# Kernel tuning notes

Measured on AMD Instinct MI355X. Metric: run time of the kernel, lower is better.

Reference implementation:

```python
import jax, jax.numpy as jnp
import numpy as np

N_HEADS = 16
HEAD_DIM = 64
N_EMBD = 1024
B, S = 2, 2048


def setup_inputs() -> dict:
    key = jax.random.key(0)
    k1, k2, k3 = jax.random.split(key, 3)
    x = jax.random.normal(k1, (B, S, N_EMBD), dtype=jnp.float32)
    W_attn = jax.random.normal(k2, (N_EMBD, 3 * N_EMBD), dtype=jnp.float32) * 0.02
    b_attn = jnp.zeros((3 * N_EMBD,), dtype=jnp.float32)
    W_proj = jax.random.normal(k3, (N_EMBD, N_EMBD), dtype=jnp.float32) * 0.02
    b_proj = jnp.zeros((N_EMBD,), dtype=jnp.float32)
    return {"x": x, "W_attn": W_attn, "b_attn": b_attn, "W_proj": W_proj, "b_proj": b_proj}


def reference(x, W_attn, b_attn, W_proj, b_proj):
    b, s, _ = x.shape
    qkv = x @ W_attn + b_attn  # (b, s, 3*n_embd)
    q, k, v = jnp.split(qkv, 3, axis=-1)
    # (b, s, n_embd) -> (b, h, s, d)
    def heads(t):
        return t.reshape(b, s, N_HEADS, HEAD_DIM).transpose(0, 2, 1, 3)
    q, k, v = heads(q), heads(k), heads(v)
    scale = 1.0 / jnp.sqrt(jnp.float32(HEAD_DIM))
    scores = jnp.einsum("bhqd,bhkd->bhqk", q, k) * scale
    causal = jnp.triu(jnp.full((s, s), -jnp.inf, dtype=scores.dtype), k=1)
    scores = scores + causal[None, None, :, :]
    attn = jax.nn.softmax(scores, axis=-1)
    out = jnp.einsum("bhqk,bhkd->bhqd", attn, v)  # (b, h, s, d)
    out = out.transpose(0, 2, 1, 3).reshape(b, s, N_EMBD)
    return out @ W_proj + b_proj
```

## Files before the change

### kernel.cpp

```cpp
#include <hip/hip_runtime.h>
#include <hip/hip_bf16.h>
#include <stdint.h>
#include <stddef.h>

typedef __bf16 bf16_t;
typedef __attribute__((ext_vector_type(8))) __bf16 bf16x8;
typedef __attribute__((ext_vector_type(4))) __bf16 bf16x4;
typedef __attribute__((ext_vector_type(4))) float f32x4;

#define MFMA_BF16(a, b, c) __builtin_amdgcn_mfma_f32_16x16x32_bf16((a), (b), (c), 0, 0, 0)

__global__ void detect_dtype(const unsigned short* __restrict__ x, int* __restrict__ flag) {
  __shared__ int cnt;
  if (threadIdx.x == 0) cnt = 0;
  __syncthreads();
  int local = 0;
  for (int i = threadIdx.x; i < 16384; i += 256) {
    const int e = (x[i] >> 7) & 0xFF;
    if (e >= 0x8D) local++;
  }
  atomicAdd(&cnt, local);
  __syncthreads();
  if (threadIdx.x == 0) *flag = (cnt > 16) ? 1 : 0;
}

__global__ void cvt_x(const float* __restrict__ in, bf16_t* __restrict__ out,
                      const int* __restrict__ flagp) {
  if (!*flagp) return;
  const size_t i = ((size_t)blockIdx.x * 256 + threadIdx.x) * 8;
  const float4 a = *(const float4*)(in + i), b = *(const float4*)(in + i + 4);
  bf16x8 r;
  r[0] = (__bf16)a.x; r[1] = (__bf16)a.y; r[2] = (__bf16)a.z; r[3] = (__bf16)a.w;
  r[4] = (__bf16)b.x; r[5] = (__bf16)b.y; r[6] = (__bf16)b.z; r[7] = (__bf16)b.w;
  *(bf16x8*)(out + i) = r;
}

__global__ void transpose_any(const void* __restrict__ in, bf16_t* __restrict__ out,
                              int R, int C, const int* __restrict__ flagp) {
  const int isF32 = *flagp;
  __shared__ bf16_t tile[32][33];
  const int tx = threadIdx.x, ty = threadIdx.y;
  const int r0 = blockIdx.y * 32, c0 = blockIdx.x * 32;
#pragma unroll
  for (int i = 0; i < 4; ++i) {
    const size_t idx = (size_t)(r0 + ty + i * 8) * C + (c0 + tx);
    tile[ty + i * 8][tx] = isF32 ? (bf16_t)((const float*)in)[idx]
                                 : ((const bf16_t*)in)[idx];
  }
  __syncthreads();
#pragma unroll
  for (int i = 0; i < 4; ++i)
    out[(size_t)(c0 + ty + i * 8) * R + (r0 + tx)] = tile[tx][ty + i * 8];
}

#define GP 72
template <int MODE>
__global__ __launch_bounds__(256) void gemm_bt(const void* A0,
                        const bf16_t* __restrict__ xb,
                        const bf16_t* __restrict__ Bt,
                        const void* __restrict__ bias,
                        void* C,
                        bf16_t* __restrict__ Qs,
                        bf16_t* __restrict__ Kb,
                        bf16_t* __restrict__ dout_bf,
                        int M, int N, int K,
                        const int* __restrict__ flagp) {
  const int isF32 = *flagp;
  const bf16_t* A = (MODE == 1 && isF32) ? xb : (const bf16_t*)A0;
  bf16_t* Vt = dout_bf + (isF32 ? (size_t)4194304 : 0);

  __shared__ __align__(16) unsigned char pool[128 * GP * 2 * 2];
  bf16_t* As = (bf16_t*)pool;
  bf16_t* Bs = (bf16_t*)pool + 128 * GP;

  const int tid = threadIdx.x;
  const int w = tid >> 6, lane = tid & 63;
  const int quad = lane >> 4, l16 = lane & 15;
  const int wm = w >> 1, wn = w & 1;
  const int m0 = blockIdx.y * 128, n0 = blockIdx.x * 128;

  auto loadA = [&](int k0, int it) -> bf16x8 {
    const int g = it * 256 + tid;
    const int row = g >> 3, col = (g & 7) * 8;
    const int m = m0 + row;
    if (MODE == 2) {
      const size_t aoff =
          ((size_t)((m >> 11) * 16 + (k0 >> 6)) * 2048 + (m & 2047)) * 64 + col;
      return *(const bf16x8*)(A + aoff);
    }
    return *(const bf16x8*)(A + (size_t)m * K + (k0 + col));
  };
  auto loadB = [&](int k0, int it) -> bf16x8 {
    const int g = it * 256 + tid;
    const int row = g >> 3, col = (g & 7) * 8;
    return *(const bf16x8*)(Bt + (size_t)(n0 + row) * K + (k0 + col));
  };

  f32x4 acc[4][4];
#pragma unroll
  for (int i = 0; i < 4; ++i)
#pragma unroll
    for (int j = 0; j < 4; ++j) acc[i][j] = f32x4{0.f, 0.f, 0.f, 0.f};

  bf16x8 va[4], vb[4];
#pragma unroll
  for (int it = 0; it < 4; ++it) { va[it] = loadA(0, it); vb[it] = loadB(0, it); }

  for (int k0 = 0; k0 < K; k0 += 64) {
    __syncthreads();
#pragma unroll
    for (int it = 0; it < 4; ++it) {
      const int g = it * 256 + tid;
      const int row = g >> 3, col = (g & 7) * 8;
      *(bf16x8*)&As[row * GP + col] = va[it];
      *(bf16x8*)&Bs[row * GP + col] = vb[it];
    }
    __syncthreads();

    if (k0 + 64 < K) {
#pragma unroll
      for (int it = 0; it < 4; ++it) { va[it] = loadA(k0 + 64, it); vb[it] = loadB(k0 + 64, it); }
    }

#pragma unroll
    for (int kc = 0; kc < 2; ++kc) {
      bf16x8 af[4], bfr[4];
#pragma unroll
      for (int i = 0; i < 4; ++i)
        af[i] = *(const bf16x8*)&As[(wm * 64 + i * 16 + l16) * GP + kc * 32 + quad * 8];
#pragma unroll
      for (int j = 0; j < 4; ++j)
        bfr[j] = *(const bf16x8*)&Bs[(wn * 64 + j * 16 + l16) * GP + kc * 32 + quad * 8];
#pragma unroll
      for (int i = 0; i < 4; ++i)
#pragma unroll
        for (int j = 0; j < 4; ++j) acc[i][j] = MFMA_BF16(af[i], bfr[j], acc[i][j]);
    }
  }

  if (MODE == 1 && n0 >= 2048) {
    bf16_t* tp = (bf16_t*)pool;
    __syncthreads();
#pragma unroll
    for (int j = 0; j < 4; ++j) {
      const int n_l = wn * 64 + j * 16 + l16;
      const int n = n0 + n_l;
      const float bj = isF32 ? ((const float*)bias)[n] : (float)((const bf16_t*)bias)[n];
#pragma unroll
      for (int i = 0; i < 4; ++i) {
#pragma unroll
        for (int r = 0; r < 4; ++r) {
          const int m_l = wm * 64 + i * 16 + quad * 4 + r;
          tp[n_l * 136 + m_l] = (bf16_t)(acc[i][j][r] + bj);
        }
      }
    }
    __syncthreads();
    const int b = m0 >> 11, s0 = m0 & 2047;
#pragma unroll
    for (int seg = 0; seg < 8; ++seg) {
      const int idx = seg * 256 + tid;
      const int n_l = idx >> 4, ms = (idx & 15) * 8;
      const bf16x8 v8 = *(const bf16x8*)&tp[n_l * 136 + ms];
      const int e = (n0 + n_l) & 1023, h = e >> 6, d = e & 63;
      *(bf16x8*)(Vt + ((size_t)(b * 16 + h) * 64 + d) * 2048 + s0 + ms) = v8;
    }
    return;
  }

#pragma unroll
  for (int j = 0; j < 4; ++j) {
    const int n = n0 + wn * 64 + j * 16 + l16;
    const float bj = isF32 ? ((const float*)bias)[n] : (float)((const bf16_t*)bias)[n];
#pragma unroll
    for (int i = 0; i < 4; ++i) {
      const int mbase = m0 + wm * 64 + i * 16 + quad * 4;
#pragma unroll
      for (int r = 0; r < 4; ++r) {
        const int m = mbase + r;
        const float v = acc[i][j][r] + bj;
        if (MODE == 2) {
          if (isF32) ((float*)C)[(size_t)m * N + n] = v;
          else       ((bf16_t*)C)[(size_t)m * N + n] = (bf16_t)v;
        } else {
          const int e = n & 1023;
          const int h = e >> 6, d = e & 63;
          const int bb = m >> 11, s = m & 2047;
          const size_t bh = (size_t)(bb * 16 + h);
          if ((n >> 10) == 0) Qs[(bh * 2048 + s) * 64 + d] = (bf16_t)(v * 0.18033688011f);
          else                Kb[(bh * 2048 + s) * 64 + d] = (bf16_t)v;
        }
      }
    }
  }
}

#define AP 72
#define PSP 72
__global__ __launch_bounds__(256, 5) void attn_kernel(bf16_t* QO,
                                                      const bf16_t* __restrict__ Kb,
                                                      const bf16_t* __restrict__ dout_bf,
                                                      const int* __restrict__ flagp) {
  const int isF32 = *flagp;
  const bf16_t* Vt = dout_bf + (isF32 ? (size_t)4194304 : 0);

  __shared__ __align__(16) bf16_t Ks[64 * AP];
  __shared__ __align__(16) bf16_t Vs[64 * AP];
  __shared__ __align__(16) bf16_t Ps[4][16 * PSP];

  const int bid = blockIdx.x;
  const int g = bid >> 5, bh = bid & 31;
  const int qt = (g < 16) ? (31 - g) : (g - 16);

  const int tid = threadIdx.x, w = tid >> 6, lane = tid & 63;
  const int quad = lane >> 4, l16 = lane & 15;

  bf16_t* Q = QO + (size_t)bh * 2048 * 64;
  const bf16_t* K = Kb + (size_t)bh * 2048 * 64;
  const bf16_t* V = Vt + (size_t)bh * 64 * 2048;

  const int qrow = qt * 64 + w * 16;
  const int nkt = qt + 1;

  bf16x8 qf[2];
#pragma unroll
  for (int kk = 0; kk < 2; ++kk)
    qf[kk] = *(const bf16x8*)(Q + (size_t)(qrow + l16) * 64 + kk * 32 + quad * 8);

  f32x4 oacc[4];
  float lsum = 0.f;
#pragma unroll
  for (int jd = 0; jd < 4; ++jd) oacc[jd] = f32x4{0.f, 0.f, 0.f, 0.f};

  const int srow8 = lane >> 3;
  const int scol8 = (lane & 7) * 8;

  auto loadK = [&](int kt, int it) -> bf16x8 {
    const int row = (w + it * 4) * 8 + srow8;
    return *(const bf16x8*)(K + (size_t)(kt * 64 + row) * 64 + scol8);
  };
  auto loadV = [&](int kt, int it) -> bf16x8 {
    const int row = (w + it * 4) * 8 + srow8;
    return *(const bf16x8*)(V + (size_t)row * 2048 + kt * 64 + scol8);
  };

  bf16x8 kv[2], vv[2];
#pragma unroll
  for (int it = 0; it < 2; ++it) { kv[it] = loadK(0, it); vv[it] = loadV(0, it); }

  for (int kt = 0; kt < nkt; ++kt) {
    __syncthreads();
#pragma unroll
    for (int it = 0; it < 2; ++it) {
      const int row = (w + it * 4) * 8 + srow8;
      *(bf16x8*)&Ks[row * AP + scol8] = kv[it];
      *(bf16x8*)&Vs[row * AP + scol8] = vv[it];
    }
    __syncthreads();

    if (kt + 1 < nkt) {
#pragma unroll
      for (int it = 0; it < 2; ++it) { kv[it] = loadK(kt + 1, it); vv[it] = loadV(kt + 1, it); }
    }

    const int kbase = kt * 64;
    f32x4 s[4];
#pragma unroll
    for (int j = 0; j < 4; ++j) {
      const bf16x8 kf0 = *(const bf16x8*)&Ks[(j * 16 + l16) * AP + quad * 8];
      const bf16x8 kf1 = *(const bf16x8*)&Ks[(j * 16 + l16) * AP + 32 + quad * 8];
      f32x4 z = f32x4{0.f, 0.f, 0.f, 0.f};
      z = MFMA_BF16(kf0, qf[0], z);
      s[j] = MFMA_BF16(kf1, qf[1], z);
    }

    if (kbase + 63 > qrow) {
      const int qg = qrow + l16;
#pragma unroll
      for (int j = 0; j < 4; ++j) {
        const int key = kbase + j * 16 + quad * 4;
#pragma unroll
        for (int r = 0; r < 4; ++r)
          if (key + r > qg) s[j][r] = -1e30f;
      }
    }

#pragma unroll
    for (int j = 0; j < 4; ++j) {
      bf16x4 pk;
#pragma unroll
      for (int r = 0; r < 4; ++r) {
        const float p = exp2f(s[j][r]);
        lsum += p;
        pk[r] = (__bf16)p;
      }
      *(bf16x4*)&Ps[w][l16 * PSP + j * 16 + quad * 4] = pk;
    }

#pragma unroll
    for (int kk = 0; kk < 2; ++kk) {
      const bf16x8 pf = *(const bf16x8*)&Ps[w][l16 * PSP + kk * 32 + quad * 8];
#pragma unroll
      for (int jd = 0; jd < 4; ++jd) {
        const bf16x8 vf = *(const bf16x8*)&Vs[(jd * 16 + l16) * AP + kk * 32 + quad * 8];
        oacc[jd] = MFMA_BF16(pf, vf, oacc[jd]);
      }
    }
  }

  lsum += __shfl_xor(lsum, 16);
  lsum += __shfl_xor(lsum, 32);

#pragma unroll
  for (int r = 0; r < 4; ++r) {
    const float lr = fmaxf(__shfl(lsum, quad * 4 + r, 16), 1e-30f);
    const int q = qrow + quad * 4 + r;
#pragma unroll
    for (int jd = 0; jd < 4; ++jd) {
      const int d = jd * 16 + l16;
      Q[(size_t)q * 64 + d] = (bf16_t)(oacc[jd][r] / lr);
    }
  }
}

extern "C" void kernel_launch(void* const* d_in, const int* in_sizes, int n_in,
                              void* d_out, int out_size, void* d_ws, size_t ws_size,
                              hipStream_t stream) {
  const void* x      = d_in[0];
  const void* W_attn = d_in[1];
  const void* b_attn = d_in[2];
  const void* W_proj = d_in[3];
  const void* b_proj = d_in[4];

  char* ws = (char*)d_ws;
  size_t off = 0;
  auto alloc = [&](size_t bytes) {
    char* p = ws + off;
    off += (bytes + 255) & ~(size_t)255;
    return p;
  };
  int*    flag = (int*)alloc(256);
  bf16_t* Qs   = (bf16_t*)alloc((size_t)32 * 2048 * 64 * 2);
  bf16_t* Kb   = (bf16_t*)alloc((size_t)32 * 2048 * 64 * 2);
  bf16_t* Wat  = (bf16_t*)alloc((size_t)3072 * 1024 * 2);
  bf16_t* Wpt  = (bf16_t*)alloc((size_t)1024 * 1024 * 2);
  bf16_t* dout_bf = (bf16_t*)d_out;

  detect_dtype<<<1, 256, 0, stream>>>((const unsigned short*)x, flag);

  cvt_x<<<2048, 256, 0, stream>>>((const float*)x, dout_bf, flag);

  transpose_any<<<dim3(3072 / 32, 1024 / 32), dim3(32, 8), 0, stream>>>(W_attn, Wat, 1024, 3072, flag);
  transpose_any<<<dim3(1024 / 32, 1024 / 32), dim3(32, 8), 0, stream>>>(W_proj, Wpt, 1024, 1024, flag);

  gemm_bt<1><<<dim3(3072 / 128, 4096 / 128), 256, 0, stream>>>(
      x, dout_bf, Wat, b_attn, nullptr, Qs, Kb, dout_bf, 4096, 3072, 1024, flag);

  attn_kernel<<<dim3(1024), 256, 0, stream>>>(Qs, Kb, dout_bf, flag);

  gemm_bt<2><<<dim3(1024 / 128, 4096 / 128), 256, 0, stream>>>(
      Qs, nullptr, Wpt, b_proj, d_out, nullptr, nullptr, dout_bf, 4096, 1024, 1024, flag);
}
```

Before: 194.6 us.

## Double-buffer GEMM register prefetch, coalesce Q/K epilogue via LDS, add MFMA priority hints

The GEMM main loop now keeps two sets of prefetch registers, so global loads for tile k+2 are issued while tile k is being computed, giving deeper latency hiding. The Q/K epilogue of the QKV projection is rewritten to stage results through shared memory and write 16-byte vectors per row, replacing scattered scalar bf16 stores. s_setprio hints are also placed around the MFMA blocks in both the GEMM and the attention kernel. The extra prefetch registers raise VGPR pressure and may reduce occupancy, and the unrolled loop assumes K is a multiple of 128.

```diff
diff --git a/kernel.cpp b/kernel.cpp
--- a/kernel.cpp
+++ b/kernel.cpp
@@ -102,12 +102,7 @@
 #pragma unroll
     for (int j = 0; j < 4; ++j) acc[i][j] = f32x4{0.f, 0.f, 0.f, 0.f};
 
-  bf16x8 va[4], vb[4];
-#pragma unroll
-  for (int it = 0; it < 4; ++it) { va[it] = loadA(0, it); vb[it] = loadB(0, it); }
-
-  for (int k0 = 0; k0 < K; k0 += 64) {
-    __syncthreads();
+  auto stage = [&](bf16x8* va, bf16x8* vb) {
 #pragma unroll
     for (int it = 0; it < 4; ++it) {
       const int g = it * 256 + tid;
@@ -115,13 +110,8 @@
       *(bf16x8*)&As[row * GP + col] = va[it];
       *(bf16x8*)&Bs[row * GP + col] = vb[it];
     }
-    __syncthreads();
-
-    if (k0 + 64 < K) {
-#pragma unroll
-      for (int it = 0; it < 4; ++it) { va[it] = loadA(k0 + 64, it); vb[it] = loadB(k0 + 64, it); }
-    }
-
+  };
+  auto compute = [&]() {
 #pragma unroll
     for (int kc = 0; kc < 2; ++kc) {
       bf16x8 af[4], bfr[4];
@@ -131,11 +121,38 @@
 #pragma unroll
       for (int j = 0; j < 4; ++j)
         bfr[j] = *(const bf16x8*)&Bs[(wn * 64 + j * 16 + l16) * GP + kc * 32 + quad * 8];
+      __builtin_amdgcn_s_setprio(1);
 #pragma unroll
       for (int i = 0; i < 4; ++i)
 #pragma unroll
         for (int j = 0; j < 4; ++j) acc[i][j] = MFMA_BF16(af[i], bfr[j], acc[i][j]);
-    }
+      __builtin_amdgcn_s_setprio(0);
+    }
+  };
+
+  bf16x8 va0[4], vb0[4], va1[4], vb1[4];
+#pragma unroll
+  for (int it = 0; it < 4; ++it) { va0[it] = loadA(0, it);  vb0[it] = loadB(0, it); }
+#pragma unroll
+  for (int it = 0; it < 4; ++it) { va1[it] = loadA(64, it); vb1[it] = loadB(64, it); }
+
+  for (int k0 = 0; k0 < K; k0 += 128) {
+    __syncthreads();
+    stage(va0, vb0);
+    __syncthreads();
+    if (k0 + 128 < K) {
+#pragma unroll
+      for (int it = 0; it < 4; ++it) { va0[it] = loadA(k0 + 128, it); vb0[it] = loadB(k0 + 128, it); }
+    }
+    compute();
+    __syncthreads();
+    stage(va1, vb1);
+    __syncthreads();
+    if (k0 + 192 < K) {
+#pragma unroll
+      for (int it = 0; it < 4; ++it) { va1[it] = loadA(k0 + 192, it); vb1[it] = loadB(k0 + 192, it); }
+    }
+    compute();
   }
 
   if (MODE == 1 && n0 >= 2048) {
@@ -168,6 +185,40 @@
     return;
   }
 
+  if (MODE == 1) {
+    bf16_t* tp = (bf16_t*)pool;
+    __syncthreads();
+    const bool isQ = (n0 < 1024);
+    const float sc = isQ ? 0.18033688011f : 1.0f;
+#pragma unroll
+    for (int j = 0; j < 4; ++j) {
+      const int n_l = wn * 64 + j * 16 + l16;
+      const int n = n0 + n_l;
+      const float bj = isF32 ? ((const float*)bias)[n] : (float)((const bf16_t*)bias)[n];
+#pragma unroll
+      for (int i = 0; i < 4; ++i) {
+#pragma unroll
+        for (int r = 0; r < 4; ++r) {
+          const int m_l = wm * 64 + i * 16 + quad * 4 + r;
+          tp[m_l * 136 + n_l] = (bf16_t)((acc[i][j][r] + bj) * sc);
+        }
+      }
+    }
+    __syncthreads();
+    bf16_t* dst = isQ ? Qs : Kb;
+#pragma unroll
+    for (int seg = 0; seg < 8; ++seg) {
+      const int idx = seg * 256 + tid;
+      const int m_l = idx >> 4, ns = (idx & 15) * 8;
+      const bf16x8 v8 = *(const bf16x8*)&tp[m_l * 136 + ns];
+      const int m = m0 + m_l;
+      const int e = (n0 + ns) & 1023, h = e >> 6, d = e & 63;
+      const int bb = m >> 11, s = m & 2047;
+      *(bf16x8*)(dst + (((size_t)(bb * 16 + h) * 2048 + s) * 64 + d)) = v8;
+    }
+    return;
+  }
+
 #pragma unroll
   for (int j = 0; j < 4; ++j) {
     const int n = n0 + wn * 64 + j * 16 + l16;
@@ -179,17 +230,8 @@
       for (int r = 0; r < 4; ++r) {
         const int m = mbase + r;
         const float v = acc[i][j][r] + bj;
-        if (MODE == 2) {
-          if (isF32) ((float*)C)[(size_t)m * N + n] = v;
-          else       ((bf16_t*)C)[(size_t)m * N + n] = (bf16_t)v;
-        } else {
-          const int e = n & 1023;
-          const int h = e >> 6, d = e & 63;
-          const int bb = m >> 11, s = m & 2047;
-          const size_t bh = (size_t)(bb * 16 + h);
-          if ((n >> 10) == 0) Qs[(bh * 2048 + s) * 64 + d] = (bf16_t)(v * 0.18033688011f);
-          else                Kb[(bh * 2048 + s) * 64 + d] = (bf16_t)v;
-        }
+        if (isF32) ((float*)C)[(size_t)m * N + n] = v;
+        else       ((bf16_t*)C)[(size_t)m * N + n] = (bf16_t)v;
       }
     }
   }
@@ -265,6 +307,7 @@
 
     const int kbase = kt * 64;
     f32x4 s[4];
+    __builtin_amdgcn_s_setprio(1);
 #pragma unroll
     for (int j = 0; j < 4; ++j) {
       const bf16x8 kf0 = *(const bf16x8*)&Ks[(j * 16 + l16) * AP + quad * 8];
@@ -273,6 +316,7 @@
       z = MFMA_BF16(kf0, qf[0], z);
       s[j] = MFMA_BF16(kf1, qf[1], z);
     }
+    __builtin_amdgcn_s_setprio(0);
 
     if (kbase + 63 > qrow) {
       const int qg = qrow + l16;
@@ -297,6 +341,7 @@
       *(bf16x4*)&Ps[w][l16 * PSP + j * 16 + quad * 4] = pk;
     }
 
+    __builtin_amdgcn_s_setprio(1);
 #pragma unroll
     for (int kk = 0; kk < 2; ++kk) {
       const bf16x8 pf = *(const bf16x8*)&Ps[w][l16 * PSP + kk * 32 + quad * 8];
@@ -306,6 +351,7 @@
         oacc[jd] = MFMA_BF16(pf, vf, oacc[jd]);
       }
     }
+    __builtin_amdgcn_s_setprio(0);
   }
 
   lsum += __shfl_xor(lsum, 16);
```

New measurement: 199.5 us. 1.03x slower.

## Switch attention to 32x32 MFMA with register-resident P via permlane swap

Applied to the files above, without the earlier changes.

Rewrites the attention kernel to use 32x32x16 bf16 MFMA with 2 waves per block, each covering 32 query rows. The probability tile is packed to bf16 and rearranged in registers with v_permlane32_swap instead of going through shared memory, which removes the Ps buffer and its LDS traffic. It trades fewer waves per block and higher register pressure for larger MFMA tiles and less LDS round-tripping. The softmax still uses no running max, so it relies on bounded scores.

```diff
diff --git a/kernel.cpp b/kernel.cpp
--- a/kernel.cpp
+++ b/kernel.cpp
@@ -5,10 +5,18 @@
 
 typedef __bf16 bf16_t;
 typedef __attribute__((ext_vector_type(8))) __bf16 bf16x8;
-typedef __attribute__((ext_vector_type(4))) __bf16 bf16x4;
 typedef __attribute__((ext_vector_type(4))) float f32x4;
+typedef __attribute__((ext_vector_type(16))) float f32x16;
+typedef __attribute__((ext_vector_type(4))) unsigned u32x4;
 
 #define MFMA_BF16(a, b, c) __builtin_amdgcn_mfma_f32_16x16x32_bf16((a), (b), (c), 0, 0, 0)
+#define MFMA32(a, b, c)    __builtin_amdgcn_mfma_f32_32x32x16_bf16((a), (b), (c), 0, 0, 0)
+
+static __device__ __forceinline__ unsigned pk2(float x, float y) {
+  const unsigned short lo = __builtin_bit_cast(unsigned short, (__bf16)x);
+  const unsigned short hi = __builtin_bit_cast(unsigned short, (__bf16)y);
+  return ((unsigned)hi << 16) | lo;
+}
 
 __global__ void detect_dtype(const unsigned short* __restrict__ x, int* __restrict__ flag) {
   __shared__ int cnt;
@@ -196,8 +204,7 @@
 }
 
 #define AP 72
-#define PSP 72
-__global__ __launch_bounds__(256, 5) void attn_kernel(bf16_t* QO,
+__global__ __launch_bounds__(128, 2) void attn_kernel(bf16_t* QO,
                                                       const bf16_t* __restrict__ Kb,
                                                       const bf16_t* __restrict__ dout_bf,
                                                       const int* __restrict__ flagp) {
@@ -206,120 +213,121 @@
 
   __shared__ __align__(16) bf16_t Ks[64 * AP];
   __shared__ __align__(16) bf16_t Vs[64 * AP];
-  __shared__ __align__(16) bf16_t Ps[4][16 * PSP];
 
   const int bid = blockIdx.x;
   const int g = bid >> 5, bh = bid & 31;
   const int qt = (g < 16) ? (31 - g) : (g - 16);
 
   const int tid = threadIdx.x, w = tid >> 6, lane = tid & 63;
-  const int quad = lane >> 4, l16 = lane & 15;
+  const int c = lane & 31, hi = lane >> 5;
 
   bf16_t* Q = QO + (size_t)bh * 2048 * 64;
   const bf16_t* K = Kb + (size_t)bh * 2048 * 64;
   const bf16_t* V = Vt + (size_t)bh * 64 * 2048;
 
-  const int qrow = qt * 64 + w * 16;
+  const int qrow = qt * 64 + w * 32;
   const int nkt = qt + 1;
 
-  bf16x8 qf[2];
-#pragma unroll
-  for (int kk = 0; kk < 2; ++kk)
-    qf[kk] = *(const bf16x8*)(Q + (size_t)(qrow + l16) * 64 + kk * 32 + quad * 8);
-
-  f32x4 oacc[4];
+  bf16x8 qf[4];
+#pragma unroll
+  for (int ks = 0; ks < 4; ++ks)
+    qf[ks] = *(const bf16x8*)(Q + (size_t)(qrow + c) * 64 + ks * 16 + hi * 8);
+
+  f32x16 oacc0 = {0,0,0,0,0,0,0,0,0,0,0,0,0,0,0,0};
+  f32x16 oacc1 = {0,0,0,0,0,0,0,0,0,0,0,0,0,0,0,0};
   float lsum = 0.f;
-#pragma unroll
-  for (int jd = 0; jd < 4; ++jd) oacc[jd] = f32x4{0.f, 0.f, 0.f, 0.f};
-
-  const int srow8 = lane >> 3;
-  const int scol8 = (lane & 7) * 8;
+
+  const int srow = tid >> 3;
+  const int scol = (tid & 7) * 8;
 
   auto loadK = [&](int kt, int it) -> bf16x8 {
-    const int row = (w + it * 4) * 8 + srow8;
-    return *(const bf16x8*)(K + (size_t)(kt * 64 + row) * 64 + scol8);
+    return *(const bf16x8*)(K + (size_t)(kt * 64 + it * 16 + srow) * 64 + scol);
   };
   auto loadV = [&](int kt, int it) -> bf16x8 {
-    const int row = (w + it * 4) * 8 + srow8;
-    return *(const bf16x8*)(V + (size_t)row * 2048 + kt * 64 + scol8);
-  };
-
-  bf16x8 kv[2], vv[2];
-#pragma unroll
-  for (int it = 0; it < 2; ++it) { kv[it] = loadK(0, it); vv[it] = loadV(0, it); }
+    return *(const bf16x8*)(V + (size_t)(it * 16 + srow) * 2048 + kt * 64 + scol);
+  };
+
+  bf16x8 kv[4], vv[4];
+#pragma unroll
+  for (int it = 0; it < 4; ++it) { kv[it] = loadK(0, it); vv[it] = loadV(0, it); }
 
   for (int kt = 0; kt < nkt; ++kt) {
     __syncthreads();
 #pragma unroll
-    for (int it = 0; it < 2; ++it) {
-      const int row = (w + it * 4) * 8 + srow8;
-      *(bf16x8*)&Ks[row * AP + scol8] = kv[it];
-      *(bf16x8*)&Vs[row * AP + scol8] = vv[it];
+    for (int it = 0; it < 4; ++it) {
+      *(bf16x8*)&Ks[(it * 16 + srow) * AP + scol] = kv[it];
+      *(bf16x8*)&Vs[(it * 16 + srow) * AP + scol] = vv[it];
     }
     __syncthreads();
 
     if (kt + 1 < nkt) {
 #pragma unroll
-      for (int it = 0; it < 2; ++it) { kv[it] = loadK(kt + 1, it); vv[it] = loadV(kt + 1, it); }
-    }
-
-    const int kbase = kt * 64;
-    f32x4 s[4];
-#pragma unroll
-    for (int j = 0; j < 4; ++j) {
-      const bf16x8 kf0 = *(const bf16x8*)&Ks[(j * 16 + l16) * AP + quad * 8];
-      const bf16x8 kf1 = *(const bf16x8*)&Ks[(j * 16 + l16) * AP + 32 + quad * 8];
-      f32x4 z = f32x4{0.f, 0.f, 0.f, 0.f};
-      z = MFMA_BF16(kf0, qf[0], z);
-      s[j] = MFMA_BF16(kf1, qf[1], z);
-    }
-
-    if (kbase + 63 > qrow) {
-      const int qg = qrow + l16;
-#pragma unroll
-      for (int j = 0; j < 4; ++j) {
-        const int key = kbase + j * 16 + quad * 4;
-#pragma unroll
-        for (int r = 0; r < 4; ++r)
-          if (key + r > qg) s[j][r] = -1e30f;
+      for (int it = 0; it < 4; ++it) { kv[it] = loadK(kt + 1, it); vv[it] = loadV(kt + 1, it); }
+    }
+
+    f32x16 s0 = {0,0,0,0,0,0,0,0,0,0,0,0,0,0,0,0};
+    f32x16 s1 = {0,0,0,0,0,0,0,0,0,0,0,0,0,0,0,0};
+#pragma unroll
+    for (int ks = 0; ks < 4; ++ks) {
+      const bf16x8 kf0 = *(const bf16x8*)&Ks[(c)      * AP + ks * 16 + hi * 8];
+      const bf16x8 kf1 = *(const bf16x8*)&Ks[(32 + c) * AP + ks * 16 + hi * 8];
+      s0 = MFMA32(kf0, qf[ks], s0);
+      s1 = MFMA32(kf1, qf[ks], s1);
+    }
+
+    if (kt * 64 + 63 > qrow) {
+      const int qg = qrow + c;
+#pragma unroll
+      for (int j = 0; j < 16; ++j) {
+        const int key = kt * 64 + (j & 3) + 8 * (j >> 2) + 4 * hi;
+        if (key > qg)      s0[j] = -1e30f;
+        if (key + 32 > qg) s1[j] = -1e30f;
       }
     }
 
-#pragma unroll
-    for (int j = 0; j < 4; ++j) {
-      bf16x4 pk;
-#pragma unroll
-      for (int r = 0; r < 4; ++r) {
-        const float p = exp2f(s[j][r]);
-        lsum += p;
-        pk[r] = (__bf16)p;
-      }
-      *(bf16x4*)&Ps[w][l16 * PSP + j * 16 + quad * 4] = pk;
-    }
-
-#pragma unroll
-    for (int kk = 0; kk < 2; ++kk) {
-      const bf16x8 pf = *(const bf16x8*)&Ps[w][l16 * PSP + kk * 32 + quad * 8];
-#pragma unroll
-      for (int jd = 0; jd < 4; ++jd) {
-        const bf16x8 vf = *(const bf16x8*)&Vs[(jd * 16 + l16) * AP + kk * 32 + quad * 8];
-        oacc[jd] = MFMA_BF16(pf, vf, oacc[jd]);
-      }
-    }
-  }
-
-  lsum += __shfl_xor(lsum, 16);
+    unsigned w0[8], w1[8];
+#pragma unroll
+    for (int t = 0; t < 8; ++t) {
+      const float p0 = exp2f(s0[2 * t]), p1 = exp2f(s0[2 * t + 1]);
+      const float r0 = exp2f(s1[2 * t]), r1 = exp2f(s1[2 * t + 1]);
+      lsum += (p0 + p1) + (r0 + r1);
+      w0[t] = pk2(p0, p1);
+      w1[t] = pk2(r0, r1);
+    }
+
+    asm volatile("v_permlane32_swap_b32 %0, %1" : "+v"(w0[0]), "+v"(w0[2]));
+    asm volatile("v_permlane32_swap_b32 %0, %1" : "+v"(w0[1]), "+v"(w0[3]));
+    asm volatile("v_permlane32_swap_b32 %0, %1" : "+v"(w0[4]), "+v"(w0[6]));
+    asm volatile("v_permlane32_swap_b32 %0, %1" : "+v"(w0[5]), "+v"(w0[7]));
+    asm volatile("v_permlane32_swap_b32 %0, %1" : "+v"(w1[0]), "+v"(w1[2]));
+    asm volatile("v_permlane32_swap_b32 %0, %1" : "+v"(w1[1]), "+v"(w1[3]));
+    asm volatile("v_permlane32_swap_b32 %0, %1" : "+v"(w1[4]), "+v"(w1[6]));
+    asm volatile("v_permlane32_swap_b32 %0, %1" : "+v"(w1[5]), "+v"(w1[7]));
+
+    const bf16x8 pa0 = __builtin_bit_cast(bf16x8, (u32x4){w0[0], w0[1], w0[2], w0[3]});
+    const bf16x8 pa1 = __builtin_bit_cast(bf16x8, (u32x4){w0[4], w0[5], w0[6], w0[7]});
+    const bf16x8 pa2 = __builtin_bit_cast(bf16x8, (u32x4){w1[0], w1[1], w1[2], w1[3]});
+    const bf16x8 pa3 = __builtin_bit_cast(bf16x8, (u32x4){w1[4], w1[5], w1[6], w1[7]});
+
+#pragma unroll
+    for (int kp = 0; kp < 4; ++kp) {
+      const bf16x8 paf = (kp == 0) ? pa0 : (kp == 1) ? pa1 : (kp == 2) ? pa2 : pa3;
+      const bf16x8 vf0 = *(const bf16x8*)&Vs[(c)      * AP + kp * 16 + hi * 8];
+      const bf16x8 vf1 = *(const bf16x8*)&Vs[(32 + c) * AP + kp * 16 + hi * 8];
+      oacc0 = MFMA32(paf, vf0, oacc0);
+      oacc1 = MFMA32(paf, vf1, oacc1);
+    }
+  }
+
   lsum += __shfl_xor(lsum, 32);
 
 #pragma unroll
-  for (int r = 0; r < 4; ++r) {
-    const float lr = fmaxf(__shfl(lsum, quad * 4 + r, 16), 1e-30f);
-    const int q = qrow + quad * 4 + r;
-#pragma unroll
-    for (int jd = 0; jd < 4; ++jd) {
-      const int d = jd * 16 + l16;
-      Q[(size_t)q * 64 + d] = (bf16_t)(oacc[jd][r] / lr);
-    }
+  for (int j = 0; j < 16; ++j) {
+    const int qloc = (j & 3) + 8 * (j >> 2) + 4 * hi;
+    const float li = fmaxf(__shfl(lsum, qloc), 1e-30f);
+    const int q = qrow + qloc;
+    Q[(size_t)q * 64 + c]      = (bf16_t)(oacc0[j] / li);
+    Q[(size_t)q * 64 + 32 + c] = (bf16_t)(oacc1[j] / li);
   }
 }
 
@@ -356,7 +364,7 @@
   gemm_bt<1><<<dim3(3072 / 128, 4096 / 128), 256, 0, stream>>>(
       x, dout_bf, Wat, b_attn, nullptr, Qs, Kb, dout_bf, 4096, 3072, 1024, flag);
 
-  attn_kernel<<<dim3(1024), 256, 0, stream>>>(Qs, Kb, dout_bf, flag);
+  attn_kernel<<<dim3(1024), 128, 0, stream>>>(Qs, Kb, dout_bf, flag);
 
   gemm_bt<2><<<dim3(1024 / 128, 4096 / 128), 256, 0, stream>>>(
       Qs, nullptr, Wpt, b_proj, d_out, nullptr, nullptr, dout_bf, 4096, 1024, 1024, flag);
```

After: 215.7 us. 1.11x slower.
